# Optimization experiments

Measured on AMD Instinct MI355X. Metric: run time of the kernel, lower is better.

The kernel has to match this reference:

```python
import jax, jax.numpy as jnp
from jax import lax
import numpy as np

B, K = 32, 8
NUM_LABELS = 600
GRID = 100          # grid_size
FEATURE_DIM = 256
HUMAN = 100         # human_width == human_height


def setup_inputs() -> dict:
    rng = np.random.default_rng(0)
    ids = rng.integers(0, NUM_LABELS, size=(B, K))
    # Synthetic OA_distn: per-label MVN params (means + Cholesky factors of small covs).
    # Means chosen so sampled obj_x/obj_y are non-negative (well-defined slicing regime).
    mean_xy = rng.uniform(0.2, 0.8, size=(NUM_LABELS, 2)).astype(np.float32)
    mean_wh = rng.uniform(-0.3, 0.3, size=(NUM_LABELS, 2)).astype(np.float32)
    L = 0.05 * np.eye(2, dtype=np.float32)  # shared Cholesky factor (cov = L L^T)
    eps_xy = rng.standard_normal((B, K, 2)).astype(np.float32)
    eps_wh = rng.standard_normal((B, K, 2)).astype(np.float32)
    d_xy = mean_xy[ids] + eps_xy @ L.T      # MVN sample per (b,k): mean + L eps
    d_wh = mean_wh[ids] + eps_wh @ L.T
    delta_x, delta_y = d_xy[..., 0], d_xy[..., 1]
    delta_w, delta_h = d_wh[..., 0], d_wh[..., 1]
    # .int() truncation as in torch
    obj_x = np.clip((delta_x * HUMAN).astype(np.int32), 0, None)
    obj_y = np.clip((delta_y * HUMAN).astype(np.int32), 0, None)
    obj_w = (HUMAN * np.exp(delta_w)).astype(np.int32)
    obj_h = (HUMAN * np.exp(delta_h)).astype(np.int32)
    # global canvas size: host-side max, mirrors .max().item()
    g_w = int(np.maximum(HUMAN, obj_x + obj_w).max())
    g_h = int(np.maximum(HUMAN, obj_y + obj_h).max())
    # learned params
    ks = jax.random.split(jax.random.key(0), 3)
    conv1_w = jax.random.normal(ks[0], (16, 2, 3, 3), jnp.float32) * 0.1
    conv1_b = jnp.zeros((16,), jnp.float32)
    conv2_w = jax.random.normal(ks[1], (32, 16, 3, 3), jnp.float32) * 0.05
    conv2_b = jnp.zeros((32,), jnp.float32)
    proj_w = jax.random.normal(ks[2], (FEATURE_DIM, 32 * GRID * GRID), jnp.float32) * 0.002
    proj_b = jnp.zeros((FEATURE_DIM,), jnp.float32)
    return {
        'obj_x': jnp.asarray(obj_x), 'obj_y': jnp.asarray(obj_y),
        'obj_w': jnp.asarray(obj_w), 'obj_h': jnp.asarray(obj_h),
        'g_h': g_h, 'g_w': g_w,
        'conv1_w': conv1_w, 'conv1_b': conv1_b,
        'conv2_w': conv2_w, 'conv2_b': conv2_b,
        'proj_w': proj_w, 'proj_b': proj_b,
    }


def _binary_maps(obj_x, obj_y, obj_w, obj_h, g_h, g_w):
    # Vectorized rectangle rasterization on the (g_h, g_w) global canvas.
    b, k = obj_x.shape
    yy = jnp.arange(g_h)[None, None, :, None]   # (1,1,gH,1)
    xx = jnp.arange(g_w)[None, None, None, :]   # (1,1,1,gW)
    human = jnp.broadcast_to(((yy < HUMAN) & (xx < HUMAN)), (b, k, g_h, g_w)).astype(jnp.float32)
    ox = obj_x[..., None, None]; oy = obj_y[..., None, None]
    ow = obj_w[..., None, None]; oh = obj_h[..., None, None]
    obj = ((yy >= oy) & (yy < oy + oh) & (xx >= ox) & (xx < ox + ow)).astype(jnp.float32)
    maps = jnp.stack((human, obj), axis=2).reshape(b * k, 2, g_h, g_w)
    # bilinear, half-pixel centers, no antialias == torch F.interpolate(align_corners=False)
    return jax.image.resize(maps, (b * k, 2, GRID, GRID), method='bilinear', antialias=False)


def reference(obj_x, obj_y, obj_w, obj_h, g_h, g_w, conv1_w, conv1_b, conv2_w, conv2_b, proj_w, proj_b):
    b, k = obj_x.shape
    maps = _binary_maps(obj_x, obj_y, obj_w, obj_h, g_h, g_w)  # (B*K,2,GRID,GRID)
    dn = ('NCHW', 'OIHW', 'NCHW')
    x = lax.conv_general_dilated(maps, conv1_w, (1, 1), 'SAME', dimension_numbers=dn) + conv1_b[None, :, None, None]
    x = lax.conv_general_dilated(x, conv2_w, (1, 1), 'SAME', dimension_numbers=dn) + conv2_b[None, :, None, None]
    x = x.reshape(b * k, -1)                     # (B*K, 32*GRID*GRID), CHW order
    out = x @ proj_w.T + proj_b                  # (B*K, FEATURE_DIM)
    return out.reshape(b, k, FEATURE_DIM)
```

## Files before the change

### kernel.cpp

```cpp
#include <hip/hip_runtime.h>
#include <cstddef>

#define NS 256
#define NF 256
#define NC1 16
#define NC2 32

__global__ __launch_bounds__(256) void k_prep(
    const int* __restrict__ obx, const int* __restrict__ oby,
    const int* __restrict__ obw, const int* __restrict__ obh,
    const int* __restrict__ ghp, const int* __restrict__ gwp,
    const float* __restrict__ w1, const float* __restrict__ w2,
    const float* __restrict__ pb,
    float* __restrict__ pyT, float* __restrict__ pxT,
    float* __restrict__ hy, float* __restrict__ hx,
    float* __restrict__ Weff, float* __restrict__ base) {
  int tid = threadIdx.x;
  if (blockIdx.x == 0) {
    int n = tid;
    float gh = (float)ghp[0], gw = (float)gwp[0];
    float sy = gh / 100.0f, sx = gw / 100.0f;
    int x0 = obx[n], y0 = oby[n], w = obw[n], h = obh[n];
    for (int j = 0; j < 100; ++j) {
      float u = (j + 0.5f) * sx - 0.5f;
      int a0 = (int)floorf(u);
      float t = u - (float)a0;
      float v0 = (a0 >= x0 && a0 < x0 + w) ? 1.f : 0.f;
      float v1 = (a0 + 1 >= x0 && a0 + 1 < x0 + w) ? 1.f : 0.f;
      pxT[j * 256 + n] = (1.f - t) * v0 + t * v1;
      u = (j + 0.5f) * sy - 0.5f;
      a0 = (int)floorf(u);
      t = u - (float)a0;
      v0 = (a0 >= y0 && a0 < y0 + h) ? 1.f : 0.f;
      v1 = (a0 + 1 >= y0 && a0 + 1 < y0 + h) ? 1.f : 0.f;
      pyT[j * 256 + n] = (1.f - t) * v0 + t * v1;
    }
    if (n < 100) {
      int j = n;
      float u = (j + 0.5f) * sx - 0.5f;
      int a0 = (int)floorf(u);
      float t = u - (float)a0;
      float v0 = (a0 >= 0 && a0 < 100) ? 1.f : 0.f;
      float v1 = (a0 + 1 >= 0 && a0 + 1 < 100) ? 1.f : 0.f;
      hx[j] = (1.f - t) * v0 + t * v1;
      u = (j + 0.5f) * sy - 0.5f;
      a0 = (int)floorf(u);
      t = u - (float)a0;
      v0 = (a0 >= 0 && a0 < 100) ? 1.f : 0.f;
      v1 = (a0 + 1 >= 0 && a0 + 1 < 100) ? 1.f : 0.f;
      hy[j] = (1.f - t) * v0 + t * v1;
    }
  } else if (blockIdx.x == 1) {
    for (int idx = tid; idx < NC2 * 25; idx += 256) {
      int c2 = idx / 25, d = idx % 25;
      int dy = d / 5, dx = d % 5;
      float s = 0.f;
      for (int c1 = 0; c1 < NC1; ++c1)
        for (int sy = 0; sy < 3; ++sy) {
          int ty = dy - sy;
          if (ty < 0 || ty > 2) continue;
          for (int sx = 0; sx < 3; ++sx) {
            int tx = dx - sx;
            if (tx < 0 || tx > 2) continue;
            s += w1[((c1 * 2 + 1) * 3 + (2 - sy)) * 3 + (2 - sx)] *
                 w2[((c2 * NC1 + c1) * 9 + (2 - ty) * 3 + (2 - tx))];
          }
        }
      Weff[idx] = s;
    }
  } else {
    base[tid] = pb[tid];
  }
}

__global__ __launch_bounds__(256) void k_t1h(
    const float* __restrict__ w1, const float* __restrict__ b1,
    const float* __restrict__ hy, const float* __restrict__ hx,
    float* __restrict__ t1h) {
  int idx = blockIdx.x * 256 + threadIdx.x;
  if (idx >= NC1 * 10000) return;
  int c1 = idx / 10000, p = idx % 10000;
  int i = p / 100, j = p % 100;
  float acc = b1[c1];
  for (int dy = 0; dy < 3; ++dy) {
    int yy = i + dy - 1;
    if (yy < 0 || yy >= 100) continue;
    for (int dx = 0; dx < 3; ++dx) {
      int xx = j + dx - 1;
      if (xx < 0 || xx >= 100) continue;
      acc += w1[((c1 * 2 + 0) * 3 + dy) * 3 + dx] * hy[yy] * hx[xx];
    }
  }
  t1h[idx] = acc;
}

__global__ __launch_bounds__(256) void k_t2h(
    const float* __restrict__ w2, const float* __restrict__ b2,
    const float* __restrict__ t1h, float* __restrict__ t2h) {
  int idx = blockIdx.x * 256 + threadIdx.x;
  if (idx >= NC2 * 10000) return;
  int c2 = idx / 10000, p = idx % 10000;
  int i = p / 100, j = p % 100;
  float acc = b2[c2];
  for (int c1 = 0; c1 < NC1; ++c1)
    for (int dy = 0; dy < 3; ++dy) {
      int yy = i + dy - 1;
      if (yy < 0 || yy >= 100) continue;
      for (int dx = 0; dx < 3; ++dx) {
        int xx = j + dx - 1;
        if (xx < 0 || xx >= 100) continue;
        acc += w2[((c2 * NC1 + c1) * 9 + dy * 3 + dx)] *
               t1h[c1 * 10000 + yy * 100 + xx];
      }
    }
  t2h[idx] = acc;
}

__global__ __launch_bounds__(256) void k_adj5(
    const float* __restrict__ P, const float* __restrict__ Weff,
    const float* __restrict__ t2h, float* __restrict__ G,
    float* __restrict__ base, float* __restrict__ rimbuf) {
  __shared__ __align__(16) float buf[2][44 * 116];
  int tid = threadIdx.x;
  int f = blockIdx.y;
  int r0 = blockIdx.x * 40;
  const float* Pf = P + (size_t)f * (NC2 * 10000);
  float* rimf = rimbuf + (size_t)f * (NC2 * 400);

  auto stage = [&](float* b, int c2) {
    const float* Pc = Pf + c2 * 10000;
    float* rimc = rimf + c2 * 400;
    for (int w = tid; w < 1100; w += 256) {
      int row = w / 25, k = w % 25;
      int gr = r0 - 2 + row;
      if (gr >= 0 && gr < 100) {
        float4 val = *(const float4*)(Pc + gr * 100 + k * 4);
        *(float4*)(b + row * 116 + 4 + k * 4) = val;
        if (gr == 0) *(float4*)(rimc + k * 4) = val;
        if (gr == 99) *(float4*)(rimc + 100 + k * 4) = val;
        if (k == 0) rimc[200 + gr] = val.x;
        if (k == 24) rimc[300 + gr] = val.w;
      }
    }
  };

  for (int i = tid; i < 2 * 44 * 116; i += 256) ((float*)buf)[i] = 0.f;
  __syncthreads();
  stage(buf[0], 0);

  int rowg = tid / 25, colg = tid % 25;
  bool act = tid < 250;
  float acc[4][4] = {};
  float bacc = 0.f;

  for (int c2 = 0; c2 < NC2; ++c2) {
    __syncthreads();
    if (c2 + 1 < NC2) stage(buf[(c2 + 1) & 1], c2 + 1);
    if (act) {
      const float* lp = &buf[c2 & 1][rowg * 464 + colg * 4];
      const float* We = Weff + c2 * 25;
#pragma unroll
      for (int ir = 0; ir < 8; ++ir) {
        float4 A = *(const float4*)(lp + ir * 116);
        float4 Bv = *(const float4*)(lp + ir * 116 + 4);
        float4 Cv = *(const float4*)(lp + ir * 116 + 8);
        float v[12] = {A.x,  A.y,  A.z,  A.w,  Bv.x, Bv.y,
                       Bv.z, Bv.w, Cv.x, Cv.y, Cv.z, Cv.w};
#pragma unroll
        for (int rr = 0; rr < 4; ++rr) {
          int dy = ir - rr;
          if (dy < 0 || dy > 4) continue;
#pragma unroll
          for (int dx = 0; dx < 5; ++dx) {
            float w = We[dy * 5 + dx];
#pragma unroll
            for (int cc = 0; cc < 4; ++cc) acc[rr][cc] += w * v[2 + dx + cc];
          }
          if (dy == 2) {
            int grow = r0 + rowg * 4 + rr;
            if (grow < 100) {
              float4 t =
                  *(const float4*)(t2h + c2 * 10000 + grow * 100 + colg * 4);
              bacc += t.x * v[4] + t.y * v[5] + t.z * v[6] + t.w * v[7];
            }
          }
        }
      }
    }
  }
  if (act) {
#pragma unroll
    for (int rr = 0; rr < 4; ++rr) {
      int grow = r0 + rowg * 4 + rr;
      if (grow < 100)
        *(float4*)&G[(size_t)f * 10000 + grow * 100 + colg * 4] =
            *(float4*)&acc[rr][0];
    }
  }
  __syncthreads();
  float* red = &buf[0][0];
  red[tid] = bacc;
  __syncthreads();
  for (int s = 128; s > 0; s >>= 1) {
    if (tid < s) red[tid] += red[tid + s];
    __syncthreads();
  }
  if (tid == 0) atomicAdd(&base[f], red[0]);
}

__global__ __launch_bounds__(256) void k_rim(
    const float* __restrict__ rimbuf, const float* __restrict__ w2,
    const float* __restrict__ w1, float* __restrict__ G) {
  __shared__ float rs[NC2 * 400];
  __shared__ float hs[NC1 * 404];
  __shared__ float w1s[288];
  int tid = threadIdx.x;
  int f = blockIdx.x;
  for (int i = tid; i < NC2 * 400; i += 256)
    rs[i] = rimbuf[(size_t)f * (NC2 * 400) + i];
  for (int i = tid; i < 288; i += 256) w1s[i] = w1[i];
  __syncthreads();
  for (int qq = 0; qq < 2; ++qq) {
    int j = tid + qq * 256;
    if (j >= 404) break;
    int qy, qx;
    if (j < 102) { qy = -1; qx = j - 1; }
    else if (j < 204) { qy = 100; qx = j - 103; }
    else if (j < 304) { qy = j - 204; qx = -1; }
    else { qy = j - 304; qx = 100; }
    float hacc[NC1];
#pragma unroll
    for (int c1 = 0; c1 < NC1; ++c1) hacc[c1] = 0.f;
#pragma unroll
    for (int ty = 0; ty < 3; ++ty)
#pragma unroll
      for (int tx = 0; tx < 3; ++tx) {
        int r = qy + ty - 1, c = qx + tx - 1;
        bool ok = (r >= 0 && r < 100 && c >= 0 && c < 100);
        int side, i2;
        if (r == 0) { side = 0; i2 = c; }
        else if (r == 99) { side = 1; i2 = c; }
        else if (c == 0) { side = 2; i2 = r; }
        else { side = 3; i2 = r; }
        i2 = min(max(i2, 0), 99);
        int rbase = side * 100 + i2;
        if (ok) {
          for (int c2 = 0; c2 < NC2; ++c2) {
            float val = rs[c2 * 400 + rbase];
#pragma unroll
            for (int c1 = 0; c1 < NC1; ++c1)
              hacc[c1] +=
                  w2[(c2 * NC1 + c1) * 9 + (2 - ty) * 3 + (2 - tx)] * val;
          }
        }
      }
#pragma unroll
    for (int c1 = 0; c1 < NC1; ++c1) hs[c1 * 404 + j] = hacc[c1];
  }
  __syncthreads();
  for (int idx = tid; idx < 396; idx += 256) {
    int py, px;
    if (idx < 100) { py = 0; px = idx; }
    else if (idx < 200) { py = 99; px = idx - 100; }
    else if (idx < 298) { py = idx - 199; px = 0; }
    else { py = idx - 297; px = 99; }
    float corr = 0.f;
    for (int sy = 0; sy < 3; ++sy)
      for (int sx = 0; sx < 3; ++sx) {
        int qy = py + sy - 1, qx = px + sx - 1;
        bool ph = (qy == -1 || qy == 100 || qx == -1 || qx == 100);
        if (!ph) continue;
        int j;
        if (qy == -1) j = qx + 1;
        else if (qy == 100) j = 103 + qx;
        else if (qx == -1) j = 204 + qy;
        else j = 304 + qy;
#pragma unroll
        for (int c1 = 0; c1 < NC1; ++c1)
          corr += w1s[((c1 * 2 + 1) * 3 + (2 - sy)) * 3 + (2 - sx)] *
                  hs[c1 * 404 + j];
      }
    G[(size_t)f * 10000 + py * 100 + px] -= corr;
  }
}

__global__ __launch_bounds__(256) void k_gemm(
    const float* __restrict__ G, const float* __restrict__ pyT,
    const float* __restrict__ pxT, float* __restrict__ part) {
  __shared__ float Gs[8 * 132];
  __shared__ float Ms[8 * 128];
  int tid = threadIdx.x;
  int fT = blockIdx.x, nT = blockIdx.y, kS = blockIdx.z;
  int f0 = fT * 128, n0 = nT * 128, kb0 = kS * 80;
  int tf = tid % 16, tn = tid / 16;
  int fG = tid >> 1, kq = (tid & 1) * 4;
  int nl = tid & 127, kh = tid >> 7;
  float acc[8][8] = {};
  for (int ch = 0; ch < 10; ++ch) {
    int kb = kb0 + ch * 8;
    __syncthreads();
    {
      float4 g = *(const float4*)&G[(size_t)(f0 + fG) * 10000 + kb + kq];
      Gs[(kq + 0) * 132 + fG] = g.x;
      Gs[(kq + 1) * 132 + fG] = g.y;
      Gs[(kq + 2) * 132 + fG] = g.z;
      Gs[(kq + 3) * 132 + fG] = g.w;
    }
#pragma unroll
    for (int kk = 0; kk < 4; ++kk) {
      int k = kh * 4 + kk;
      int p = kb + k;
      int pi = p / 100, pj = p - pi * 100;
      Ms[k * 128 + nl] = pyT[pi * 256 + n0 + nl] * pxT[pj * 256 + n0 + nl];
    }
    __syncthreads();
#pragma unroll
    for (int k = 0; k < 8; ++k) {
      float4 ga = *(const float4*)&Gs[k * 132 + tf * 4];
      float4 gb = *(const float4*)&Gs[k * 132 + 64 + tf * 4];
      float4 ma = *(const float4*)&Ms[k * 128 + tn * 8];
      float4 mb = *(const float4*)&Ms[k * 128 + tn * 8 + 4];
      float gv[8] = {ga.x, ga.y, ga.z, ga.w, gb.x, gb.y, gb.z, gb.w};
      float mv[8] = {ma.x, ma.y, ma.z, ma.w, mb.x, mb.y, mb.z, mb.w};
#pragma unroll
      for (int nn = 0; nn < 8; ++nn)
#pragma unroll
        for (int ff = 0; ff < 8; ++ff) acc[nn][ff] += mv[nn] * gv[ff];
    }
  }
  size_t pb = (((size_t)kS * 2 + nT) * 2 + fT) * 16384;
#pragma unroll
  for (int nn = 0; nn < 8; ++nn) {
    int row = tn * 8 + nn;
    *(float4*)&part[pb + row * 128 + tf * 4] =
        make_float4(acc[nn][0], acc[nn][1], acc[nn][2], acc[nn][3]);
    *(float4*)&part[pb + row * 128 + 64 + tf * 4] =
        make_float4(acc[nn][4], acc[nn][5], acc[nn][6], acc[nn][7]);
  }
}

__global__ __launch_bounds__(256) void k_out(
    const float* __restrict__ part, const float* __restrict__ base,
    float* __restrict__ out) {
  int gid = blockIdx.x * 256 + threadIdx.x;
  int f = gid & 255, n = gid >> 8;
  int nT = n >> 7, nl = n & 127, fT = f >> 7, fl = f & 127;
  float val = base[f];
  size_t off = ((size_t)(nT * 2 + fT)) * 16384 + nl * 128 + fl;
  for (int s = 0; s < 125; ++s) val += part[(size_t)s * 65536 + off];
  out[(size_t)n * 256 + f] = val;
}

extern "C" void kernel_launch(void* const* d_in, const int* in_sizes, int n_in,
                              void* d_out, int out_size, void* d_ws,
                              size_t ws_size, hipStream_t stream) {
  const int* obj_x = (const int*)d_in[0];
  const int* obj_y = (const int*)d_in[1];
  const int* obj_w = (const int*)d_in[2];
  const int* obj_h = (const int*)d_in[3];
  const int* g_h = (const int*)d_in[4];
  const int* g_w = (const int*)d_in[5];
  const float* conv1_w = (const float*)d_in[6];
  const float* conv1_b = (const float*)d_in[7];
  const float* conv2_w = (const float*)d_in[8];
  const float* conv2_b = (const float*)d_in[9];
  const float* proj_w = (const float*)d_in[10];
  const float* proj_b = (const float*)d_in[11];
  float* out = (float*)d_out;

  float* w = (float*)d_ws;
  float* pyT = w;    w += 100 * 256;
  float* pxT = w;    w += 100 * 256;
  float* hy = w;     w += 100;
  float* hx = w;     w += 100;
  float* t1h = w;    w += NC1 * 10000;
  float* t2h = w;    w += NC2 * 10000;
  float* base = w;   w += NF;
  float* Weff = w;   w += NC2 * 25;
  float* G = w;      w += (size_t)NF * 10000;
  float* rimbuf = w; w += (size_t)NF * NC2 * 400;
  float* part = w;   w += (size_t)500 * 16384;

  k_prep<<<3, 256, 0, stream>>>(obj_x, obj_y, obj_w, obj_h, g_h, g_w, conv1_w,
                                conv2_w, proj_b, pyT, pxT, hy, hx, Weff, base);
  k_t1h<<<625, 256, 0, stream>>>(conv1_w, conv1_b, hy, hx, t1h);
  k_t2h<<<1250, 256, 0, stream>>>(conv2_w, conv2_b, t1h, t2h);
  k_adj5<<<dim3(3, 256), 256, 0, stream>>>(proj_w, Weff, t2h, G, base, rimbuf);
  k_rim<<<256, 256, 0, stream>>>(rimbuf, conv2_w, conv1_w, G);
  k_gemm<<<dim3(2, 2, 125), 256, 0, stream>>>(G, pyT, pxT, part);
  k_out<<<256, 256, 0, stream>>>(part, base, out);
}
```

Baseline: 755.6 us.

## Fuse human-map conv kernels via shared memory and retile adjoint conv

```diff
diff --git a/kernel.cpp b/kernel.cpp
--- a/kernel.cpp
+++ b/kernel.cpp
@@ -73,54 +73,76 @@
   }
 }
 
-__global__ __launch_bounds__(256) void k_t1h(
+__global__ __launch_bounds__(256) void k_t2h(
     const float* __restrict__ w1, const float* __restrict__ b1,
+    const float* __restrict__ w2, const float* __restrict__ b2,
     const float* __restrict__ hy, const float* __restrict__ hx,
-    float* __restrict__ t1h) {
-  int idx = blockIdx.x * 256 + threadIdx.x;
-  if (idx >= NC1 * 10000) return;
-  int c1 = idx / 10000, p = idx % 10000;
-  int i = p / 100, j = p % 100;
-  float acc = b1[c1];
-  for (int dy = 0; dy < 3; ++dy) {
-    int yy = i + dy - 1;
-    if (yy < 0 || yy >= 100) continue;
-    for (int dx = 0; dx < 3; ++dx) {
-      int xx = j + dx - 1;
-      if (xx < 0 || xx >= 100) continue;
-      acc += w1[((c1 * 2 + 0) * 3 + dy) * 3 + dx] * hy[yy] * hx[xx];
-    }
-  }
-  t1h[idx] = acc;
-}
-
-__global__ __launch_bounds__(256) void k_t2h(
-    const float* __restrict__ w2, const float* __restrict__ b2,
-    const float* __restrict__ t1h, float* __restrict__ t2h) {
-  int idx = blockIdx.x * 256 + threadIdx.x;
-  if (idx >= NC2 * 10000) return;
-  int c2 = idx / 10000, p = idx % 10000;
-  int i = p / 100, j = p % 100;
-  float acc = b2[c2];
-  for (int c1 = 0; c1 < NC1; ++c1)
-    for (int dy = 0; dy < 3; ++dy) {
-      int yy = i + dy - 1;
-      if (yy < 0 || yy >= 100) continue;
-      for (int dx = 0; dx < 3; ++dx) {
-        int xx = j + dx - 1;
-        if (xx < 0 || xx >= 100) continue;
-        acc += w2[((c2 * NC1 + c1) * 9 + dy * 3 + dx)] *
-               t1h[c1 * 10000 + yy * 100 + xx];
-      }
-    }
-  t2h[idx] = acc;
+    float* __restrict__ t2h) {
+  __shared__ float t1s[NC1 * 3 * 104];
+  __shared__ float hxs[104];
+  __shared__ float hys[8];
+  int tid = threadIdx.x;
+  int row0 = blockIdx.x;
+  int c2 = blockIdx.y * 8 + (tid >> 5);
+  int colg = tid & 31;
+
+  if (tid < 104) {
+    int c = tid - 2;
+    hxs[tid] = (c >= 0 && c < 100) ? hx[c] : 0.f;
+  }
+  if (tid >= 104 && tid < 109) {
+    int d = tid - 104;
+    int r = row0 - 2 + d;
+    hys[d] = (r >= 0 && r < 100) ? hy[r] : 0.f;
+  }
+  __syncthreads();
+  for (int i = tid; i < NC1 * 3 * 104; i += 256) {
+    int c1 = i / 312, rem = i - c1 * 312;
+    int r = rem / 104, j = rem - r * 104;
+    int yy = row0 + r - 1, jc = j - 1;
+    float val = 0.f;
+    if (yy >= 0 && yy < 100 && jc >= 0 && jc < 100) {
+      val = b1[c1];
+#pragma unroll
+      for (int dy = 0; dy < 3; ++dy) {
+        float hv = hys[r + dy];
+#pragma unroll
+        for (int dx = 0; dx < 3; ++dx)
+          val += w1[((c1 * 2 + 0) * 3 + dy) * 3 + dx] * hv * hxs[j + dx];
+      }
+    }
+    t1s[i] = val;
+  }
+  __syncthreads();
+  if (colg < 25) {
+    float acc[4];
+    float bb = b2[c2];
+#pragma unroll
+    for (int cc = 0; cc < 4; ++cc) acc[cc] = bb;
+    for (int c1 = 0; c1 < NC1; ++c1)
+#pragma unroll
+      for (int r = 0; r < 3; ++r) {
+        const float* tp = &t1s[(c1 * 3 + r) * 104 + colg * 4];
+        float t0 = tp[0], t1 = tp[1], t2 = tp[2], t3 = tp[3], t4 = tp[4],
+              t5 = tp[5];
+#pragma unroll
+        for (int dx = 0; dx < 3; ++dx) {
+          float wv = w2[(c2 * NC1 + c1) * 9 + r * 3 + dx];
+          float tv[6] = {t0, t1, t2, t3, t4, t5};
+#pragma unroll
+          for (int cc = 0; cc < 4; ++cc) acc[cc] += wv * tv[cc + dx];
+        }
+      }
+    *(float4*)&t2h[c2 * 10000 + row0 * 100 + colg * 4] =
+        make_float4(acc[0], acc[1], acc[2], acc[3]);
+  }
 }
 
 __global__ __launch_bounds__(256) void k_adj5(
     const float* __restrict__ P, const float* __restrict__ Weff,
     const float* __restrict__ t2h, float* __restrict__ G,
     float* __restrict__ base, float* __restrict__ rimbuf) {
-  __shared__ __align__(16) float buf[2][44 * 116];
+  __shared__ __align__(16) float buf[2][44 * 112];
   int tid = threadIdx.x;
   int f = blockIdx.y;
   int r0 = blockIdx.x * 40;
@@ -130,12 +152,12 @@
   auto stage = [&](float* b, int c2) {
     const float* Pc = Pf + c2 * 10000;
     float* rimc = rimf + c2 * 400;
-    for (int w = tid; w < 1100; w += 256) {
-      int row = w / 25, k = w % 25;
+    for (int w = tid; w < 44 * 32; w += 256) {
+      int row = w >> 5, k = w & 31;
       int gr = r0 - 2 + row;
-      if (gr >= 0 && gr < 100) {
+      if (k < 25 && gr >= 0 && gr < 100) {
         float4 val = *(const float4*)(Pc + gr * 100 + k * 4);
-        *(float4*)(b + row * 116 + 4 + k * 4) = val;
+        *(float4*)(b + row * 112 + 4 + k * 4) = val;
         if (gr == 0) *(float4*)(rimc + k * 4) = val;
         if (gr == 99) *(float4*)(rimc + 100 + k * 4) = val;
         if (k == 0) rimc[200 + gr] = val.x;
@@ -144,30 +166,30 @@
     }
   };
 
-  for (int i = tid; i < 2 * 44 * 116; i += 256) ((float*)buf)[i] = 0.f;
+  for (int i = tid; i < 2 * 44 * 112; i += 256) ((float*)buf)[i] = 0.f;
   __syncthreads();
   stage(buf[0], 0);
 
-  int rowg = tid / 25, colg = tid % 25;
-  bool act = tid < 250;
-  float acc[4][4] = {};
+  int colg = tid & 31, rowg = tid >> 5;
+  bool act = (colg < 25) && (r0 + rowg * 5 < 100);
+  float acc[5][4] = {};
   float bacc = 0.f;
 
   for (int c2 = 0; c2 < NC2; ++c2) {
     __syncthreads();
     if (c2 + 1 < NC2) stage(buf[(c2 + 1) & 1], c2 + 1);
     if (act) {
-      const float* lp = &buf[c2 & 1][rowg * 464 + colg * 4];
+      const float* lp = &buf[c2 & 1][(rowg * 5) * 112 + colg * 4];
       const float* We = Weff + c2 * 25;
 #pragma unroll
-      for (int ir = 0; ir < 8; ++ir) {
-        float4 A = *(const float4*)(lp + ir * 116);
-        float4 Bv = *(const float4*)(lp + ir * 116 + 4);
-        float4 Cv = *(const float4*)(lp + ir * 116 + 8);
+      for (int ir = 0; ir < 9; ++ir) {
+        float4 A = *(const float4*)(lp + ir * 112);
+        float4 Bv = *(const float4*)(lp + ir * 112 + 4);
+        float4 Cv = *(const float4*)(lp + ir * 112 + 8);
         float v[12] = {A.x,  A.y,  A.z,  A.w,  Bv.x, Bv.y,
                        Bv.z, Bv.w, Cv.x, Cv.y, Cv.z, Cv.w};
 #pragma unroll
-        for (int rr = 0; rr < 4; ++rr) {
+        for (int rr = 0; rr < 5; ++rr) {
           int dy = ir - rr;
           if (dy < 0 || dy > 4) continue;
 #pragma unroll
@@ -177,12 +199,10 @@
             for (int cc = 0; cc < 4; ++cc) acc[rr][cc] += w * v[2 + dx + cc];
           }
           if (dy == 2) {
-            int grow = r0 + rowg * 4 + rr;
-            if (grow < 100) {
-              float4 t =
-                  *(const float4*)(t2h + c2 * 10000 + grow * 100 + colg * 4);
-              bacc += t.x * v[4] + t.y * v[5] + t.z * v[6] + t.w * v[7];
-            }
+            int grow = r0 + rowg * 5 + rr;
+            float4 t =
+                *(const float4*)(t2h + c2 * 10000 + grow * 100 + colg * 4);
+            bacc += t.x * v[4] + t.y * v[5] + t.z * v[6] + t.w * v[7];
           }
         }
       }
@@ -190,11 +210,10 @@
   }
   if (act) {
 #pragma unroll
-    for (int rr = 0; rr < 4; ++rr) {
-      int grow = r0 + rowg * 4 + rr;
-      if (grow < 100)
-        *(float4*)&G[(size_t)f * 10000 + grow * 100 + colg * 4] =
-            *(float4*)&acc[rr][0];
+    for (int rr = 0; rr < 5; ++rr) {
+      int grow = r0 + rowg * 5 + rr;
+      *(float4*)&G[(size_t)f * 10000 + grow * 100 + colg * 4] =
+          *(float4*)&acc[rr][0];
     }
   }
   __syncthreads();
@@ -373,7 +392,6 @@
   float* pxT = w;    w += 100 * 256;
   float* hy = w;     w += 100;
   float* hx = w;     w += 100;
-  float* t1h = w;    w += NC1 * 10000;
   float* t2h = w;    w += NC2 * 10000;
   float* base = w;   w += NF;
   float* Weff = w;   w += NC2 * 25;
@@ -383,8 +401,8 @@
 
   k_prep<<<3, 256, 0, stream>>>(obj_x, obj_y, obj_w, obj_h, g_h, g_w, conv1_w,
                                 conv2_w, proj_b, pyT, pxT, hy, hx, Weff, base);
-  k_t1h<<<625, 256, 0, stream>>>(conv1_w, conv1_b, hy, hx, t1h);
-  k_t2h<<<1250, 256, 0, stream>>>(conv2_w, conv2_b, t1h, t2h);
+  k_t2h<<<dim3(100, 4), 256, 0, stream>>>(conv1_w, conv1_b, conv2_w, conv2_b,
+                                          hy, hx, t2h);
   k_adj5<<<dim3(3, 256), 256, 0, stream>>>(proj_w, Weff, t2h, G, base, rimbuf);
   k_rim<<<256, 256, 0, stream>>>(rimbuf, conv2_w, conv1_w, G);
   k_gemm<<<dim3(2, 2, 125), 256, 0, stream>>>(G, pyT, pxT, part);
```

Measured after the change: 717.4 us. -5.1%, faster.
